# Performance work log

Measured on AMD Instinct MI355X. Metric: run time of the kernel, lower is better.

The kernel has to match this reference:

```python
import jax, jax.numpy as jnp
import numpy as np

B, T, C, H = 8, 1024, 768, 12
D = C // H  # head_dim = 64

def _rope_tables(seq_len, d, base=10000.0):
    inv_freq = 1.0 / (base ** (jnp.arange(0, d, 2, dtype=jnp.float32) / d))  # [d/2]
    freqs = jnp.outer(jnp.arange(seq_len, dtype=jnp.float32), inv_freq)      # [T, d/2]
    return jnp.cos(freqs), jnp.sin(freqs)

def _apply_rotary(x, cos, sin):
    # x: [B,T,H,D]; cos/sin: [1,T,1,D/2]
    d = x.shape[-1] // 2
    x1, x2 = x[..., :d], x[..., d:]
    return jnp.concatenate([x1 * cos + x2 * sin, -x1 * sin + x2 * cos], axis=-1)

def setup_inputs() -> dict:
    key = jax.random.key(0)
    k1, k2, k3 = jax.random.split(key, 3)
    x = jax.random.normal(k1, (B, T, C), dtype=jnp.float32)
    w_qkv = jax.random.normal(k2, (3 * C, C), dtype=jnp.float32) * (C ** -0.5)
    w_proj = jax.random.normal(k3, (C, C), dtype=jnp.float32) * (C ** -0.5)
    return {"x": x, "w_qkv": w_qkv, "w_proj": w_proj}

def reference(x, w_qkv, w_proj):
    Bb, Tt, Cc = x.shape
    qkv = x @ w_qkv.T                                   # [B,T,3C]
    q, k, v = jnp.split(qkv, 3, axis=2)
    q = q.reshape(Bb, Tt, H, D)
    k = k.reshape(Bb, Tt, H, D)
    v = v.reshape(Bb, Tt, H, D)
    cos, sin = _rope_tables(Tt, D)
    cos = cos[None, :, None, :]
    sin = sin[None, :, None, :]
    q = _apply_rotary(q, cos, sin)
    k = _apply_rotary(k, cos, sin)
    scale = 1.0 / jnp.sqrt(jnp.float32(D))
    scores = jnp.einsum('bthd,bshd->bhts', q, k) * scale  # [B,H,T,T]
    causal = jnp.tril(jnp.ones((Tt, Tt), dtype=bool))
    scores = jnp.where(causal[None, None], scores, jnp.finfo(scores.dtype).min)
    p = jax.nn.softmax(scores, axis=-1)
    y = jnp.einsum('bhts,bshd->bthd', p, v).reshape(Bb, Tt, Cc)
    return y @ w_proj.T
```

## Files before the change

### kernel.cpp

```cpp
#include <hip/hip_runtime.h>
#include <hip/hip_bf16.h>

#define Bb 8
#define Tt 1024
#define Cc 768
#define Hh 12
#define Dd 64
#define M_ROWS (Bb * Tt)
#define QKV_N (3 * Cc)

typedef __attribute__((ext_vector_type(8))) short s16x8;
typedef __attribute__((ext_vector_type(4))) short s16x4;
typedef __attribute__((ext_vector_type(4))) float f32x4;

#define AS1 __attribute__((address_space(1)))
#define AS3 __attribute__((address_space(3)))

template <int V> struct IC { static constexpr int value = V; };

static __device__ __forceinline__ short f2bf(float f) {
    union { float f; unsigned u; } v; v.f = f;
    unsigned r = (v.u + 0x7fffu + ((v.u >> 16) & 1u)) >> 16;
    return (short)r;
}
static __device__ __forceinline__ unsigned pkt(float hi, float lo) {
    union { float f; unsigned u; } a, b; a.f = hi; b.f = lo;
    return __builtin_amdgcn_perm(a.u, b.u, 0x07060302u);
}

static __device__ __forceinline__ void cast8(const float* __restrict__ in,
                                             short* __restrict__ out, int i) {
    const float4 a = ((const float4*)in)[i * 2];
    const float4 b = ((const float4*)in)[i * 2 + 1];
    s16x8 f;
    f[0] = f2bf(a.x); f[1] = f2bf(a.y); f[2] = f2bf(a.z); f[3] = f2bf(a.w);
    f[4] = f2bf(b.x); f[5] = f2bf(b.y); f[6] = f2bf(b.z); f[7] = f2bf(b.w);
    ((s16x8*)out)[i] = f;
}

#define S1 (M_ROWS * Cc / 8)
#define S2 (QKV_N * Cc / 8)
#define S3 (Cc * Cc / 8)
#define SROPE (Tt * 32)
#define PREP_THREADS (S1 + S2 + S3 + SROPE)

__global__ __launch_bounds__(256) void prep_kernel(const float* __restrict__ x,
                                                   const float* __restrict__ wqkv,
                                                   const float* __restrict__ wproj,
                                                   short* __restrict__ xb,
                                                   short* __restrict__ wqkvb,
                                                   short* __restrict__ wprojb,
                                                   float2* __restrict__ cs) {
    int idx = blockIdx.x * blockDim.x + threadIdx.x;
    if (idx < S1) { cast8(x, xb, idx); return; }
    idx -= S1;
    if (idx < S2) {
        int row = idx / 96;
        int c8  = idx - row * 96;
        int q2 = (row >> 4) & 3;
        int src = (row < 2 * Cc && (q2 == 1 || q2 == 2)) ? (row ^ 0x30) : row;
        const float4 a = ((const float4*)(wqkv + (size_t)src * Cc))[c8 * 2];
        const float4 b = ((const float4*)(wqkv + (size_t)src * Cc))[c8 * 2 + 1];
        s16x8 f;
        f[0] = f2bf(a.x); f[1] = f2bf(a.y); f[2] = f2bf(a.z); f[3] = f2bf(a.w);
        f[4] = f2bf(b.x); f[5] = f2bf(b.y); f[6] = f2bf(b.z); f[7] = f2bf(b.w);
        ((s16x8*)wqkvb)[idx] = f;
        return;
    }
    idx -= S2;
    if (idx < S3) { cast8(wproj, wprojb, idx); return; }
    idx -= S3;
    {
        int t = idx >> 5, i = idx & 31;
        float inv_freq = exp2f(-0.41524101186092037f * (float)i);
        float fr = (float)t * inv_freq;
        float2 v; v.x = cosf(fr); v.y = sinf(fr);
        cs[idx] = v;
    }
}

template <int MODE, int TN>
__global__ __launch_bounds__(256, 3) void gemm_nt_mfma(const short* __restrict__ A,
                                                       const short* __restrict__ B,
                                                       void* __restrict__ Cout,
                                                       const float2* __restrict__ cs,
                                                       int M, int N, int K, int nblocks) {
    __shared__ short As[2][128 * 32];
    __shared__ short Bs[2][TN * 32];
    constexpr int NTW = TN / 32;

    const int wave = threadIdx.x >> 6;
    const int lane = threadIdx.x & 63;
    const int l16  = lane & 15;
    const int quad = lane >> 4;
    const int wr = wave >> 1;
    const int wc = wave & 1;

    const int mb8  = (M >> 7) >> 3;
    const int xcd  = blockIdx.x & 7;
    const int slot = blockIdx.x >> 3;
    const int bm = (xcd * mb8 + slot / nblocks) * 128;
    const int bn = (slot % nblocks) * TN;

    f32x4 acc[4][NTW] = {};

    auto stage = [&](int k0, int buf) {
#pragma unroll
        for (int j = 0; j < 2; j++) {
            const int D = j * 256 + wave * 64 + lane;
            const int G = D >> 3;
            const int s = (G << 3) | ((D & 7) ^ (G & 7));
            const int m = s >> 2, c4 = (s & 3) * 8;
            __builtin_amdgcn_global_load_lds(
                (const AS1 unsigned*)(A + (size_t)(bm + m) * K + k0 + c4),
                (AS3 unsigned*)&As[buf][(j * 256 + wave * 64) * 8], 16, 0, 0);
        }
        constexpr int BCH = TN * 4;
#pragma unroll
        for (int j = 0; j < (BCH + 255) / 256; j++) {
            if (BCH % 256 == 0 || j * 256 + wave * 64 < BCH) {
                const int D = j * 256 + wave * 64 + lane;
                const int G = D >> 3;
                const int s = (G << 3) | ((D & 7) ^ (G & 7));
                const int m = s >> 2, c4 = (s & 3) * 8;
                __builtin_amdgcn_global_load_lds(
                    (const AS1 unsigned*)(B + (size_t)(bn + m) * K + k0 + c4),
                    (AS3 unsigned*)&Bs[buf][(j * 256 + wave * 64) * 8], 16, 0, 0);
            }
        }
    };

    const int nIter = K >> 5;
    stage(0, 0);
    for (int kt = 0; kt < nIter; kt++) {
        const int buf = kt & 1;
        __syncthreads();
        if (kt + 1 < nIter) stage((kt + 1) << 5, buf ^ 1);

        s16x8 af[4];
#pragma unroll
        for (int mt = 0; mt < 4; mt++) {
            const int m = wr * 64 + mt * 16 + l16;
            const int d = ((m & 1) * 4 + quad) ^ ((m >> 1) & 7);
            af[mt] = *(const s16x8*)&As[buf][(m >> 1) * 64 + d * 8];
        }
#pragma unroll
        for (int nt = 0; nt < NTW; nt++) {
            const int n = wc * (TN / 2) + nt * 16 + l16;
            const int d = ((n & 1) * 4 + quad) ^ ((n >> 1) & 7);
            s16x8 bf = *(const s16x8*)&Bs[buf][(n >> 1) * 64 + d * 8];
#pragma unroll
            for (int mt = 0; mt < 4; mt++)
                acc[mt][nt] = __builtin_amdgcn_mfma_f32_16x16x32_bf16(
                    af[mt], bf, acc[mt][nt], 0, 0, 0);
        }
    }

    if constexpr (MODE == 0) {
#pragma unroll
        for (int mt = 0; mt < 4; mt++)
#pragma unroll
            for (int r = 0; r < 4; r++) {
                const size_t row = bm + wr * 64 + mt * 16 + quad * 4 + r;
#pragma unroll
                for (int nt = 0; nt < NTW; nt++)
                    ((float*)Cout)[row * N + bn + wc * (TN / 2) + nt * 16 + l16] =
                        acc[mt][nt][r];
            }
    } else {
        const bool is_v = (bn >= 2 * Cc);
        if (is_v) {
#pragma unroll
            for (int mt = 0; mt < 4; mt++)
#pragma unroll
                for (int r = 0; r < 4; r++) {
                    const size_t row = bm + wr * 64 + mt * 16 + quad * 4 + r;
#pragma unroll
                    for (int nt = 0; nt < NTW; nt++)
                        ((short*)Cout)[row * N + bn + wc * (TN / 2) + nt * 16 + l16] =
                            f2bf(acc[mt][nt][r]);
                }
        } else {
            const float scale = (bn < Cc) ? 0.125f : 1.0f;
#pragma unroll
            for (int mt = 0; mt < 4; mt++) {
#pragma unroll
                for (int r = 0; r < 4; r++) {
                    const int row = bm + wr * 64 + mt * 16 + quad * 4 + r;
                    const int t = row & (Tt - 1);
                    short* cp = (short*)Cout + (size_t)row * N + bn + wc * (TN / 2);
#pragma unroll
                    for (int p = 0; p < NTW; p += 2) {
                        const int g = wc * NTW + p;
                        const int i0 = ((g & 2) ? 16 : 0) + l16;
                        const float2 c0 = cs[t * 32 + i0];
                        const float x1 = acc[mt][p][r];
                        const float x2 = acc[mt][p + 1][r];
                        cp[p * 16 + l16]        = f2bf((x1 * c0.x + x2 * c0.y) * scale);
                        cp[(p + 1) * 16 + l16]  = f2bf((-x1 * c0.y + x2 * c0.x) * scale);
                    }
                }
            }
        }
    }
}

#define QBM 128
#define QBN 288

__global__ __launch_bounds__(256, 2) void qkv_gemm_v3(const short* __restrict__ A,
                                                      const short* __restrict__ Bw,
                                                      short* __restrict__ Cq,
                                                      const float2* __restrict__ cs) {
    __shared__ short As[3][QBM * 32];
    __shared__ short Bs[3][QBN * 32];

    const int tid  = threadIdx.x;
    const int wave = tid >> 6;
    const int lane = tid & 63;
    const int l16  = lane & 15;
    const int quad = lane >> 4;
    const int wr   = wave >> 1;
    const int wc   = wave & 1;

    const int xcd  = blockIdx.x & 7;
    const int slot = blockIdx.x >> 3;
    const int bm   = (xcd * 8 + (slot >> 3)) * QBM;
    const int bn   = (slot & 7) * QBN;
    const int gt0  = (slot & 7) * 18;

    int aoff0, boffR;
    {
        const int G = tid >> 3;
        const int s = (G << 3) | ((tid & 7) ^ (G & 7));
        aoff0 = (s >> 2) * Cc + (s & 3) * 8;
    }
    {
        const int D = 1024 + (wave & 1) * 64 + lane;
        const int G = D >> 3;
        const int s = (G << 3) | ((D & 7) ^ (G & 7));
        boffR = (s >> 2) * Cc + (s & 3) * 8;
    }
    const short* Ag = A + (size_t)bm * Cc;
    const short* Bg = Bw + (size_t)bn * Cc;

    const int mA = wr * 64 + l16;
    const int abase = (mA >> 1) * 128 + ((((mA & 1) * 4 + quad) ^ ((mA >> 1) & 7)) * 16);
    const int nB = wc * 144 + l16;
    const int bbase = (nB >> 1) * 128 + ((((nB & 1) * 4 + quad) ^ ((nB >> 1) & 7)) * 16);

    f32x4 acc[4][9] = {};

#define STG_A(J, SB, K0) __builtin_amdgcn_global_load_lds(                    \
        (const AS1 unsigned*)(Ag + aoff0 + (J) * (64 * Cc) + (K0)),           \
        (AS3 unsigned*)&As[SB][((J) * 256 + wave * 64) * 8], 16, 0, 0)
#define STG_B(J, SB, K0) __builtin_amdgcn_global_load_lds(                    \
        (const AS1 unsigned*)(Bg + aoff0 + (J) * (64 * Cc) + (K0)),           \
        (AS3 unsigned*)&Bs[SB][((J) * 256 + wave * 64) * 8], 16, 0, 0)
#define STG_BR(SB, K0) __builtin_amdgcn_global_load_lds(                      \
        (const AS1 unsigned*)(Bg + boffR + (K0)),                             \
        (AS3 unsigned*)&Bs[SB][(1024 + (wave & 1) * 64) * 8], 16, 0, 0)
#define STG_ALL(SB, K0) do { STG_A(0, SB, K0); STG_A(1, SB, K0);              \
        STG_B(0, SB, K0); STG_B(1, SB, K0); STG_B(2, SB, K0);                 \
        STG_B(3, SB, K0); STG_BR(SB, K0); } while (0)

    STG_ALL(0, 0);
    STG_ALL(1, 32);
    asm volatile("s_waitcnt vmcnt(7)" ::: "memory");
    __builtin_amdgcn_s_barrier();
    asm volatile("" ::: "memory");

    int buf = 0;
    for (int kt = 0; kt < 24; kt++) {
        const int sb  = (buf == 0) ? 2 : buf - 1;
        const int k0n = (kt + 2) << 5;
        const char* ap = (const char*)&As[buf][0];
        const char* bp = (const char*)&Bs[buf][0];

        if (kt < 22) STG_ALL(sb, k0n);

        s16x8 bf[9];
#pragma unroll
        for (int nt = 0; nt < 9; nt++)
            bf[nt] = *(const s16x8*)(bp + bbase + nt * 1024);
        {
            s16x8 a0 = *(const s16x8*)(ap + abase);
            s16x8 a1 = *(const s16x8*)(ap + abase + 1024);
            __builtin_amdgcn_s_setprio(1);
#pragma unroll
            for (int nt = 0; nt < 9; nt++) {
                acc[0][nt] = __builtin_amdgcn_mfma_f32_16x16x32_bf16(a0, bf[nt], acc[0][nt], 0, 0, 0);
                acc[1][nt] = __builtin_amdgcn_mfma_f32_16x16x32_bf16(a1, bf[nt], acc[1][nt], 0, 0, 0);
            }
            __builtin_amdgcn_s_setprio(0);
        }
        {
            s16x8 a2 = *(const s16x8*)(ap + abase + 2048);
            s16x8 a3 = *(const s16x8*)(ap + abase + 3072);
            __builtin_amdgcn_s_setprio(1);
#pragma unroll
            for (int nt = 0; nt < 9; nt++) {
                acc[2][nt] = __builtin_amdgcn_mfma_f32_16x16x32_bf16(a2, bf[nt], acc[2][nt], 0, 0, 0);
                acc[3][nt] = __builtin_amdgcn_mfma_f32_16x16x32_bf16(a3, bf[nt], acc[3][nt], 0, 0, 0);
            }
            __builtin_amdgcn_s_setprio(0);
        }
        if (kt < 23) {
            if (kt <= 21) asm volatile("s_waitcnt vmcnt(7)" ::: "memory");
            else          asm volatile("s_waitcnt vmcnt(0)" ::: "memory");
            __builtin_amdgcn_s_barrier();
            asm volatile("" ::: "memory");
        }
        buf = (buf == 2) ? 0 : buf + 1;
    }

    float* scr = (float*)&As[0][0];
    if (wc == 0) {
#pragma unroll
        for (int mt = 0; mt < 4; mt++)
#pragma unroll
            for (int r = 0; r < 4; r++)
                scr[((wr * 4 + mt) * 16 + quad * 4 + r) * 16 + l16] = acc[mt][8][r];
    } else {
#pragma unroll
        for (int mt = 0; mt < 4; mt++)
#pragma unroll
            for (int r = 0; r < 4; r++)
                scr[(((2 + wr) * 4 + mt) * 16 + quad * 4 + r) * 16 + l16] = acc[mt][0][r];
    }
    __syncthreads();

    auto write_epi = [&](auto WCC) {
        constexpr int WC = decltype(WCC)::value;
        constexpr int PO = WC ? 0 : 8;
#pragma unroll
        for (int mt = 0; mt < 4; mt++) {
#pragma unroll
            for (int r = 0; r < 4; r++) {
                const int row = bm + wr * 64 + mt * 16 + quad * 4 + r;
                const int t = row & (Tt - 1);
                short* cp = Cq + (size_t)row * QKV_N + bn + WC * 144;
#pragma unroll
                for (int pp = 0; pp < 4; pp++) {
                    constexpr int PBASE = WC;
                    const int p = PBASE + 2 * pp;
                    const int g = gt0 + WC * 9 + p;
                    float x1, x2;
                    switch (pp) {
                        case 0: x1 = acc[mt][PBASE + 0][r]; x2 = acc[mt][PBASE + 1][r]; break;
                        case 1: x1 = acc[mt][PBASE + 2][r]; x2 = acc[mt][PBASE + 3][r]; break;
                        case 2: x1 = acc[mt][PBASE + 4][r]; x2 = acc[mt][PBASE + 5][r]; break;
                        default: x1 = acc[mt][PBASE + 6][r]; x2 = acc[mt][PBASE + 7][r]; break;
                    }
                    if (g < 96) {
                        const int i0 = ((g & 2) ? 16 : 0) + l16;
                        const float2 c0 = cs[t * 32 + i0];
                        const float sc = (g < 48) ? 0.125f : 1.0f;
                        cp[p * 16 + l16]       = f2bf((x1 * c0.x + x2 * c0.y) * sc);
                        cp[(p + 1) * 16 + l16] = f2bf((-x1 * c0.y + x2 * c0.x) * sc);
                    } else {
                        cp[p * 16 + l16]       = f2bf(x1);
                        cp[(p + 1) * 16 + l16] = f2bf(x2);
                    }
                }
                const float xo = acc[mt][PO][r];
                const float xp = scr[((((WC ^ 1) * 2 + wr) * 4 + mt) * 16 + quad * 4 + r) * 16 + l16];
                const int ge = gt0 + 8;
                if constexpr (WC == 0) {
                    if (ge < 96) {
                        const int i0 = ((ge & 2) ? 16 : 0) + l16;
                        const float2 c0 = cs[t * 32 + i0];
                        const float sc = (ge < 48) ? 0.125f : 1.0f;
                        cp[8 * 16 + l16] = f2bf((xo * c0.x + xp * c0.y) * sc);
                    } else {
                        cp[8 * 16 + l16] = f2bf(xo);
                    }
                } else {
                    if (ge < 96) {
                        const int i0 = ((ge & 2) ? 16 : 0) + l16;
                        const float2 c0 = cs[t * 32 + i0];
                        const float sc = (ge < 48) ? 0.125f : 1.0f;
                        cp[l16] = f2bf((-xp * c0.y + xo * c0.x) * sc);
                    } else {
                        cp[l16] = f2bf(xo);
                    }
                }
            }
        }
    };
    if (wc == 0) write_epi(IC<0>{});
    else         write_epi(IC<1>{});
#undef STG_A
#undef STG_B
#undef STG_BR
#undef STG_ALL
}

#define KSP 72
#define VSP 72

__global__ __launch_bounds__(256, 3) void flash_attn(const short* __restrict__ qkv,
                                                     short* __restrict__ y) {
    __shared__ short Ks[2][64 * KSP];
    __shared__ short Vs[2][64 * VSP];

    const int wave = threadIdx.x >> 6;
    const int lane = threadIdx.x & 63;
    const int l16  = lane & 15;
    const int quad = lane >> 4;

    const int pair = blockIdx.x / 96;
    const int bh   = blockIdx.x % 96;
    const int h = bh % Hh;
    const int b = bh / Hh;
    const int qa_blk = pair;
    const int qb_blk = 15 - pair;
    const int q0a = qa_blk * 64 + wave * 16;
    const int q0b = qb_blk * 64 + wave * 16;

    s16x8 qfa[2], qfb[2];
    {
        const short* qpa = qkv + (size_t)(b * Tt + q0a + l16) * QKV_N + h * Dd + quad * 8;
        const short* qpb = qkv + (size_t)(b * Tt + q0b + l16) * QKV_N + h * Dd + quad * 8;
        qfa[0] = *(const s16x8*)qpa;  qfa[1] = *(const s16x8*)(qpa + 32);
        qfb[0] = *(const s16x8*)qpb;  qfb[1] = *(const s16x8*)(qpb + 32);
    }

    f32x4 oa[4] = {}, ob[4] = {};
    float la = 0.f, lb = 0.f;

    const int krow = threadIdx.x >> 2;
    const int kd0  = (threadIdx.x & 3) * 16;
    const int key2 = (threadIdx.x & 31) * 2;
    const int dv0  = (threadIdx.x >> 5) * 8;

    s16x8 pk0, pk1, pv0, pv1;
    auto load_tile = [&](int kbase) {
        const short* kp = qkv + (size_t)(b * Tt + kbase + krow) * QKV_N + Cc + h * Dd + kd0;
        pk0 = *(const s16x8*)kp;
        pk1 = *(const s16x8*)(kp + 8);
        const short* vp = qkv + (size_t)(b * Tt + kbase + key2) * QKV_N + 2 * Cc + h * Dd + dv0;
        pv0 = *(const s16x8*)vp;
        pv1 = *(const s16x8*)(vp + QKV_N);
    };
    auto store_tile = [&](int buf) {
        *(s16x8*)&Ks[buf][krow * KSP + kd0]     = pk0;
        *(s16x8*)&Ks[buf][krow * KSP + kd0 + 8] = pk1;
#pragma unroll
        for (int j = 0; j < 8; j++) {
            ushort2 w; w.x = (unsigned short)pv0[j]; w.y = (unsigned short)pv1[j];
            *(ushort2*)&Vs[buf][(dv0 + j) * VSP + key2] = w;
        }
    };

    auto process_pair = [&](int buf, int kbase, bool mask_a) {
        short* pwb = &Ks[buf ^ 1][wave * 16 * KSP];
        short* pwa = &Vs[buf ^ 1][wave * 16 * VSP];
        f32x4 eb[4], ea[4];
#pragma unroll
        for (int g = 0; g < 4; g++) {
            s16x8 kf0 = *(const s16x8*)&Ks[buf][(g * 16 + l16) * KSP + quad * 8];
            s16x8 kf1 = *(const s16x8*)&Ks[buf][(g * 16 + l16) * KSP + 32 + quad * 8];
            f32x4 zb = {}, za = {};
            zb = __builtin_amdgcn_mfma_f32_16x16x32_bf16(kf0, qfb[0], zb, 0, 0, 0);
            zb = __builtin_amdgcn_mfma_f32_16x16x32_bf16(kf1, qfb[1], zb, 0, 0, 0);
            za = __builtin_amdgcn_mfma_f32_16x16x32_bf16(kf0, qfa[0], za, 0, 0, 0);
            za = __builtin_amdgcn_mfma_f32_16x16x32_bf16(kf1, qfa[1], za, 0, 0, 0);
            eb[g] = zb; ea[g] = za;
        }
        float rsb = 0.f, rsa = 0.f;
#pragma unroll
        for (int g = 0; g < 4; g++) {
#pragma unroll
            for (int r = 0; r < 4; r++) {
                float pb = __expf(eb[g][r]); rsb += pb; eb[g][r] = pb;
                float pa = __expf(ea[g][r]);
                if (mask_a) pa = (kbase + g * 16 + quad * 4 + r <= q0a + l16) ? pa : 0.0f;
                rsa += pa; ea[g][r] = pa;
            }
            uint2 ub, ua;
            ub.x = pkt(eb[g][1], eb[g][0]); ub.y = pkt(eb[g][3], eb[g][2]);
            ua.x = pkt(ea[g][1], ea[g][0]); ua.y = pkt(ea[g][3], ea[g][2]);
            *(uint2*)&pwb[l16 * KSP + g * 16 + quad * 4] = ub;
            *(uint2*)&pwa[l16 * VSP + g * 16 + quad * 4] = ua;
        }
        lb += rsb; la += rsa;
#pragma unroll
        for (int c = 0; c < 2; c++) {
            s16x8 pbb = *(const s16x8*)&pwb[l16 * KSP + c * 32 + quad * 8];
            s16x8 pba = *(const s16x8*)&pwa[l16 * VSP + c * 32 + quad * 8];
#pragma unroll
            for (int nc = 0; nc < 4; nc++) {
                s16x8 vb = *(const s16x8*)&Vs[buf][(nc * 16 + l16) * VSP + c * 32 + quad * 8];
                ob[nc] = __builtin_amdgcn_mfma_f32_16x16x32_bf16(vb, pbb, ob[nc], 0, 0, 0);
                oa[nc] = __builtin_amdgcn_mfma_f32_16x16x32_bf16(vb, pba, oa[nc], 0, 0, 0);
            }
        }
    };

    auto process_single = [&](int buf, int kbase, bool masked) {
        short* pw = &Ks[buf ^ 1][wave * 16 * KSP];
        f32x4 e[4];
#pragma unroll
        for (int g = 0; g < 4; g++) {
            s16x8 kf0 = *(const s16x8*)&Ks[buf][(g * 16 + l16) * KSP + quad * 8];
            s16x8 kf1 = *(const s16x8*)&Ks[buf][(g * 16 + l16) * KSP + 32 + quad * 8];
            f32x4 z = {};
            z = __builtin_amdgcn_mfma_f32_16x16x32_bf16(kf0, qfb[0], z, 0, 0, 0);
            z = __builtin_amdgcn_mfma_f32_16x16x32_bf16(kf1, qfb[1], z, 0, 0, 0);
            e[g] = z;
        }
        float rs = 0.f;
#pragma unroll
        for (int g = 0; g < 4; g++) {
#pragma unroll
            for (int r = 0; r < 4; r++) {
                float p = __expf(e[g][r]);
                if (masked) p = (kbase + g * 16 + quad * 4 + r <= q0b + l16) ? p : 0.0f;
                rs += p; e[g][r] = p;
            }
            uint2 u;
            u.x = pkt(e[g][1], e[g][0]); u.y = pkt(e[g][3], e[g][2]);
            *(uint2*)&pw[l16 * KSP + g * 16 + quad * 4] = u;
        }
        lb += rs;
#pragma unroll
        for (int c = 0; c < 2; c++) {
            s16x8 pb = *(const s16x8*)&pw[l16 * KSP + c * 32 + quad * 8];
#pragma unroll
            for (int nc = 0; nc < 4; nc++) {
                s16x8 vb = *(const s16x8*)&Vs[buf][(nc * 16 + l16) * VSP + c * 32 + quad * 8];
                ob[nc] = __builtin_amdgcn_mfma_f32_16x16x32_bf16(vb, pb, ob[nc], 0, 0, 0);
            }
        }
    };

    load_tile(0);
    store_tile(0);
    for (int kt = 0; kt <= qb_blk; kt++) {
        __syncthreads();
        const int nb = (kt < qb_blk) ? (kt + 1) * 64 : qb_blk * 64;
        load_tile(nb);
        const int buf = kt & 1;
        const int kbase = kt * 64;
        if (kt <= qa_blk)
            process_pair(buf, kbase, kt == qa_blk);
        else
            process_single(buf, kbase, kt == qb_blk);
        store_tile(buf ^ 1);
    }

    float sa = la; sa += __shfl_xor(sa, 16, 64); sa += __shfl_xor(sa, 32, 64);
    float sb = lb; sb += __shfl_xor(sb, 16, 64); sb += __shfl_xor(sb, 32, 64);
    const float inva = 1.0f / sa;
    const float invb = 1.0f / sb;
    short* ypa = y + (size_t)(b * Tt + q0a + l16) * Cc + h * Dd + quad * 4;
    short* ypb = y + (size_t)(b * Tt + q0b + l16) * Cc + h * Dd + quad * 4;
#pragma unroll
    for (int nc = 0; nc < 4; nc++) {
        s16x4 va, vb2;
#pragma unroll
        for (int r = 0; r < 4; r++) {
            va[r]  = f2bf(oa[nc][r] * inva);
            vb2[r] = f2bf(ob[nc][r] * invb);
        }
        *(s16x4*)&ypa[nc * 16] = va;
        *(s16x4*)&ypb[nc * 16] = vb2;
    }
}

extern "C" void kernel_launch(void* const* d_in, const int* in_sizes, int n_in,
                              void* d_out, int out_size, void* d_ws, size_t ws_size,
                              hipStream_t stream) {
    const float* x      = (const float*)d_in[0];
    const float* w_qkv  = (const float*)d_in[1];
    const float* w_proj = (const float*)d_in[2];
    float* out = (float*)d_out;

    float2* cs    = (float2*)d_ws;
    short* xb     = (short*)(cs + Tt * 32);
    short* wqkvb  = xb + (size_t)M_ROWS * Cc;
    short* wprojb = wqkvb + (size_t)QKV_N * Cc;
    short* qkvb   = wprojb + (size_t)Cc * Cc;
    short* yb     = qkvb + (size_t)M_ROWS * QKV_N;

    prep_kernel<<<PREP_THREADS / 256, 256, 0, stream>>>(
        x, w_qkv, w_proj, xb, wqkvb, wprojb, cs);

    qkv_gemm_v3<<<512, 256, 0, stream>>>(xb, wqkvb, qkvb, cs);

    flash_attn<<<96 * 8, 256, 0, stream>>>(qkvb, yb);

    gemm_nt_mfma<0, 96><<<512, 256, 0, stream>>>(
        yb, wprojb, out, nullptr, M_ROWS, Cc, Cc, Cc / 96);
}
```

Before: 177.0 us.

## Enlarge QKV GEMM to 512-thread 256-row tiles with split staging and barriers

The QKV projection GEMM now uses 256x288 tiles with 8 waves per block (512 threads, one block per CU) instead of 128-row tiles with 4 waves. Global-to-LDS staging is split into two groups interleaved with the two MFMA phases, and extra barriers plus sched_barrier keep waves in lockstep in a ping-pong style schedule. The aim is more B-tile reuse and better overlap of loads with MFMA, at the cost of lower occupancy and more barrier overhead. The flash attention kernel also raises wave priority around its MFMA sections.

```diff
diff --git a/kernel.cpp b/kernel.cpp
--- a/kernel.cpp
+++ b/kernel.cpp
@@ -205,13 +205,13 @@
     }
 }
 
-#define QBM 128
+#define QBM 256
 #define QBN 288
 
-__global__ __launch_bounds__(256, 2) void qkv_gemm_v3(const short* __restrict__ A,
-                                                      const short* __restrict__ Bw,
-                                                      short* __restrict__ Cq,
-                                                      const float2* __restrict__ cs) {
+__global__ __launch_bounds__(512, 1) void qkv_gemm_fine(const short* __restrict__ A,
+                                                        const short* __restrict__ Bw,
+                                                        short* __restrict__ Cq,
+                                                        const float2* __restrict__ cs) {
     __shared__ short As[3][QBM * 32];
     __shared__ short Bs[3][QBN * 32];
 
@@ -225,7 +225,7 @@
 
     const int xcd  = blockIdx.x & 7;
     const int slot = blockIdx.x >> 3;
-    const int bm   = (xcd * 8 + (slot >> 3)) * QBM;
+    const int bm   = (xcd * 4 + (slot >> 3)) * QBM;
     const int bn   = (slot & 7) * QBN;
     const int gt0  = (slot & 7) * 18;
 
@@ -252,68 +252,71 @@
     f32x4 acc[4][9] = {};
 
 #define STG_A(J, SB, K0) __builtin_amdgcn_global_load_lds(                    \
-        (const AS1 unsigned*)(Ag + aoff0 + (J) * (64 * Cc) + (K0)),           \
-        (AS3 unsigned*)&As[SB][((J) * 256 + wave * 64) * 8], 16, 0, 0)
+        (const AS1 unsigned*)(Ag + aoff0 + (J) * (128 * Cc) + (K0)),          \
+        (AS3 unsigned*)&As[SB][((J) * 512 + wave * 64) * 8], 16, 0, 0)
 #define STG_B(J, SB, K0) __builtin_amdgcn_global_load_lds(                    \
-        (const AS1 unsigned*)(Bg + aoff0 + (J) * (64 * Cc) + (K0)),           \
-        (AS3 unsigned*)&Bs[SB][((J) * 256 + wave * 64) * 8], 16, 0, 0)
+        (const AS1 unsigned*)(Bg + aoff0 + (J) * (128 * Cc) + (K0)),          \
+        (AS3 unsigned*)&Bs[SB][((J) * 512 + wave * 64) * 8], 16, 0, 0)
 #define STG_BR(SB, K0) __builtin_amdgcn_global_load_lds(                      \
         (const AS1 unsigned*)(Bg + boffR + (K0)),                             \
         (AS3 unsigned*)&Bs[SB][(1024 + (wave & 1) * 64) * 8], 16, 0, 0)
-#define STG_ALL(SB, K0) do { STG_A(0, SB, K0); STG_A(1, SB, K0);              \
-        STG_B(0, SB, K0); STG_B(1, SB, K0); STG_B(2, SB, K0);                 \
-        STG_B(3, SB, K0); STG_BR(SB, K0); } while (0)
-
-    STG_ALL(0, 0);
-    STG_ALL(1, 32);
-    asm volatile("s_waitcnt vmcnt(7)" ::: "memory");
-    __builtin_amdgcn_s_barrier();
-    asm volatile("" ::: "memory");
+
+#define FENCE() asm volatile("" ::: "memory")
+#define BAR()   do { FENCE(); __builtin_amdgcn_s_barrier(); FENCE(); } while (0)
+
+    STG_A(0, 0, 0);  STG_A(1, 0, 0);  STG_B(0, 0, 0);  STG_B(1, 0, 0);  STG_BR(0, 0);
+    STG_A(0, 1, 32); STG_A(1, 1, 32); STG_B(0, 1, 32); STG_B(1, 1, 32); STG_BR(1, 32);
+    asm volatile("s_waitcnt vmcnt(5)" ::: "memory");
+    BAR();
 
     int buf = 0;
     for (int kt = 0; kt < 24; kt++) {
         const int sb  = (buf == 0) ? 2 : buf - 1;
         const int k0n = (kt + 2) << 5;
+        const bool st = (kt < 22);
         const char* ap = (const char*)&As[buf][0];
         const char* bp = (const char*)&Bs[buf][0];
 
-        if (kt < 22) STG_ALL(sb, k0n);
-
+        if (st) { STG_A(0, sb, k0n); STG_A(1, sb, k0n); STG_B(0, sb, k0n); }
         s16x8 bf[9];
 #pragma unroll
         for (int nt = 0; nt < 9; nt++)
             bf[nt] = *(const s16x8*)(bp + bbase + nt * 1024);
-        {
-            s16x8 a0 = *(const s16x8*)(ap + abase);
-            s16x8 a1 = *(const s16x8*)(ap + abase + 1024);
-            __builtin_amdgcn_s_setprio(1);
-#pragma unroll
-            for (int nt = 0; nt < 9; nt++) {
-                acc[0][nt] = __builtin_amdgcn_mfma_f32_16x16x32_bf16(a0, bf[nt], acc[0][nt], 0, 0, 0);
-                acc[1][nt] = __builtin_amdgcn_mfma_f32_16x16x32_bf16(a1, bf[nt], acc[1][nt], 0, 0, 0);
-            }
-            __builtin_amdgcn_s_setprio(0);
-        }
-        {
-            s16x8 a2 = *(const s16x8*)(ap + abase + 2048);
-            s16x8 a3 = *(const s16x8*)(ap + abase + 3072);
-            __builtin_amdgcn_s_setprio(1);
-#pragma unroll
-            for (int nt = 0; nt < 9; nt++) {
-                acc[2][nt] = __builtin_amdgcn_mfma_f32_16x16x32_bf16(a2, bf[nt], acc[2][nt], 0, 0, 0);
-                acc[3][nt] = __builtin_amdgcn_mfma_f32_16x16x32_bf16(a3, bf[nt], acc[3][nt], 0, 0, 0);
-            }
-            __builtin_amdgcn_s_setprio(0);
-        }
+        s16x8 a0 = *(const s16x8*)(ap + abase);
+        s16x8 a1 = *(const s16x8*)(ap + abase + 1024);
+        BAR();
+        __builtin_amdgcn_sched_barrier(0);
+        __builtin_amdgcn_s_setprio(1);
+#pragma unroll
+        for (int nt = 0; nt < 9; nt++) {
+            acc[0][nt] = __builtin_amdgcn_mfma_f32_16x16x32_bf16(a0, bf[nt], acc[0][nt], 0, 0, 0);
+            acc[1][nt] = __builtin_amdgcn_mfma_f32_16x16x32_bf16(a1, bf[nt], acc[1][nt], 0, 0, 0);
+        }
+        __builtin_amdgcn_s_setprio(0);
+        BAR();
+
+        if (st) { STG_B(1, sb, k0n); STG_BR(sb, k0n); }
+        s16x8 a2 = *(const s16x8*)(ap + abase + 2048);
+        s16x8 a3 = *(const s16x8*)(ap + abase + 3072);
+        BAR();
+        __builtin_amdgcn_sched_barrier(0);
+        __builtin_amdgcn_s_setprio(1);
+#pragma unroll
+        for (int nt = 0; nt < 9; nt++) {
+            acc[2][nt] = __builtin_amdgcn_mfma_f32_16x16x32_bf16(a2, bf[nt], acc[2][nt], 0, 0, 0);
+            acc[3][nt] = __builtin_amdgcn_mfma_f32_16x16x32_bf16(a3, bf[nt], acc[3][nt], 0, 0, 0);
+        }
+        __builtin_amdgcn_s_setprio(0);
+
         if (kt < 23) {
-            if (kt <= 21) asm volatile("s_waitcnt vmcnt(7)" ::: "memory");
+            if (kt <= 21) asm volatile("s_waitcnt vmcnt(5)" ::: "memory");
             else          asm volatile("s_waitcnt vmcnt(0)" ::: "memory");
-            __builtin_amdgcn_s_barrier();
-            asm volatile("" ::: "memory");
+            BAR();
         }
         buf = (buf == 2) ? 0 : buf + 1;
     }
 
+    __syncthreads();
     float* scr = (float*)&As[0][0];
     if (wc == 0) {
 #pragma unroll
@@ -326,7 +329,7 @@
         for (int mt = 0; mt < 4; mt++)
 #pragma unroll
             for (int r = 0; r < 4; r++)
-                scr[(((2 + wr) * 4 + mt) * 16 + quad * 4 + r) * 16 + l16] = acc[mt][0][r];
+                scr[(((4 + wr) * 4 + mt) * 16 + quad * 4 + r) * 16 + l16] = acc[mt][0][r];
     }
     __syncthreads();
 
@@ -364,7 +367,7 @@
                     }
                 }
                 const float xo = acc[mt][PO][r];
-                const float xp = scr[((((WC ^ 1) * 2 + wr) * 4 + mt) * 16 + quad * 4 + r) * 16 + l16];
+                const float xp = scr[((((WC ^ 1) * 4 + wr) * 4 + mt) * 16 + quad * 4 + r) * 16 + l16];
                 const int ge = gt0 + 8;
                 if constexpr (WC == 0) {
                     if (ge < 96) {
@@ -393,7 +396,8 @@
 #undef STG_A
 #undef STG_B
 #undef STG_BR
-#undef STG_ALL
+#undef FENCE
+#undef BAR
 }
 
 #define KSP 72
@@ -457,6 +461,7 @@
         short* pwb = &Ks[buf ^ 1][wave * 16 * KSP];
         short* pwa = &Vs[buf ^ 1][wave * 16 * VSP];
         f32x4 eb[4], ea[4];
+        __builtin_amdgcn_s_setprio(1);
 #pragma unroll
         for (int g = 0; g < 4; g++) {
             s16x8 kf0 = *(const s16x8*)&Ks[buf][(g * 16 + l16) * KSP + quad * 8];
@@ -468,6 +473,7 @@
             za = __builtin_amdgcn_mfma_f32_16x16x32_bf16(kf1, qfa[1], za, 0, 0, 0);
             eb[g] = zb; ea[g] = za;
         }
+        __builtin_amdgcn_s_setprio(0);
         float rsb = 0.f, rsa = 0.f;
 #pragma unroll
         for (int g = 0; g < 4; g++) {
@@ -485,6 +491,7 @@
             *(uint2*)&pwa[l16 * VSP + g * 16 + quad * 4] = ua;
         }
         lb += rsb; la += rsa;
+        __builtin_amdgcn_s_setprio(1);
 #pragma unroll
         for (int c = 0; c < 2; c++) {
             s16x8 pbb = *(const s16x8*)&pwb[l16 * KSP + c * 32 + quad * 8];
@@ -496,11 +503,13 @@
                 oa[nc] = __builtin_amdgcn_mfma_f32_16x16x32_bf16(vb, pba, oa[nc], 0, 0, 0);
             }
         }
+        __builtin_amdgcn_s_setprio(0);
     };
 
     auto process_single = [&](int buf, int kbase, bool masked) {
         short* pw = &Ks[buf ^ 1][wave * 16 * KSP];
         f32x4 e[4];
+        __builtin_amdgcn_s_setprio(1);
 #pragma unroll
         for (int g = 0; g < 4; g++) {
             s16x8 kf0 = *(const s16x8*)&Ks[buf][(g * 16 + l16) * KSP + quad * 8];
@@ -510,6 +519,7 @@
             z = __builtin_amdgcn_mfma_f32_16x16x32_bf16(kf1, qfb[1], z, 0, 0, 0);
             e[g] = z;
         }
+        __builtin_amdgcn_s_setprio(0);
         float rs = 0.f;
 #pragma unroll
         for (int g = 0; g < 4; g++) {
@@ -524,6 +534,7 @@
             *(uint2*)&pw[l16 * KSP + g * 16 + quad * 4] = u;
         }
         lb += rs;
+        __builtin_amdgcn_s_setprio(1);
 #pragma unroll
         for (int c = 0; c < 2; c++) {
             s16x8 pb = *(const s16x8*)&pw[l16 * KSP + c * 32 + quad * 8];
@@ -533,6 +544,7 @@
                 ob[nc] = __builtin_amdgcn_mfma_f32_16x16x32_bf16(vb, pb, ob[nc], 0, 0, 0);
             }
         }
+        __builtin_amdgcn_s_setprio(0);
     };
 
     load_tile(0);
@@ -587,7 +599,7 @@
     prep_kernel<<<PREP_THREADS / 256, 256, 0, stream>>>(
         x, w_qkv, w_proj, xb, wqkvb, wprojb, cs);
 
-    qkv_gemm_v3<<<512, 256, 0, stream>>>(xb, wqkvb, qkvb, cs);
+    qkv_gemm_fine<<<256, 512, 0, stream>>>(xb, wqkvb, qkvb, cs);
 
     flash_attn<<<96 * 8, 256, 0, stream>>>(qkvb, yb);
 
```

Result: no change. 178.2 us (+0.7%).
